# Kernel optimization log

Measured on AMD Instinct MI355X. Metric: run time of the kernel, lower is better.

The kernel has to match this reference:

```python
import jax, jax.numpy as jnp
import numpy as np

CLASSES = 10000
SMOOTHING = 0.1
COMPLEMENT = 1.0 - SMOOTHING
GAMMA = 3.0
IGNORE_INDEX = -1


def setup_inputs() -> dict:
    key = jax.random.key(0)
    k1, k2 = jax.random.split(key)
    B, S, C = 16, 512, CLASSES
    logits = jax.random.normal(k1, (B, S, C), dtype=jnp.float32)
    target = jax.random.randint(k2, (B, S), 0, C, dtype=jnp.int64)
    return {"logits": logits, "target": target}


def reference(logits, target):
    # logits: [B, S, C], target: [B, S]
    mask = (target != IGNORE_INDEX)
    safe_t = jnp.where(mask, target, 0)
    # label smoothing: one_hot * (1 - smoothing) + smoothing / C
    oh = jax.nn.one_hot(safe_t, CLASSES, dtype=logits.dtype)
    smooth = oh * COMPLEMENT + SMOOTHING / CLASSES
    logs = jax.nn.log_softmax(logits, axis=-1)          # [B, S, C]
    pt = jnp.exp(logs)
    # focal-weighted smoothed cross-entropy per token
    per_tok = -jnp.sum((1.0 - pt) ** GAMMA * logs * smooth, axis=-1)  # [B, S]
    # mean over non-ignored tokens (matches masked-select then .mean())
    maskf = mask.astype(per_tok.dtype)
    return jnp.sum(per_tok * maskf) / jnp.sum(maskf)
```

## Files before the change

### kernel.cpp

```cpp
#include <hip/hip_runtime.h>
#include <math.h>

#define NCLASSES   10000
#define NCLASSES4  2500
#define NT         512
#define PT         5
#define IGNORE_INDEX (-1)

#define SMOOTH_UNIF  1e-5f
#define SMOOTH_COMPL 0.9f

__device__ __forceinline__ float blk_max(float v, float* red) {
    #pragma unroll
    for (int off = 32; off > 0; off >>= 1)
        v = fmaxf(v, __shfl_down(v, off, 64));
    if ((threadIdx.x & 63) == 0) red[threadIdx.x >> 6] = v;
    __syncthreads();
    if (threadIdx.x == 0) {
        float r = red[0];
        #pragma unroll
        for (int j = 1; j < NT / 64; j++) r = fmaxf(r, red[j]);
        red[0] = r;
    }
    __syncthreads();
    return red[0];
}

__device__ __forceinline__ float blk_sum(float v, float* red) {
    #pragma unroll
    for (int off = 32; off > 0; off >>= 1)
        v += __shfl_down(v, off, 64);
    if ((threadIdx.x & 63) == 0) red[threadIdx.x >> 6] = v;
    __syncthreads();
    if (threadIdx.x == 0) {
        float r = red[0];
        #pragma unroll
        for (int j = 1; j < NT / 64; j++) r += red[j];
        red[0] = r;
    }
    __syncthreads();
    return red[0];
}

__global__ __launch_bounds__(NT)
void focal_ce_token_kernel(const float* __restrict__ logits,
                           const int* __restrict__ target,
                           float* __restrict__ tok_loss,
                           float* __restrict__ tok_mask) {
    const int row = blockIdx.x;
    const int t = threadIdx.x;
    const float4* __restrict__ xrow4 =
        reinterpret_cast<const float4*>(logits + (size_t)row * NCLASSES);
    const int tgt = target[row];

    __shared__ float redA[NT / 64], redB[NT / 64], redC[NT / 64];
    __shared__ float s_xt;
    if (t == 0) s_xt = 0.0f;

    float4 v[PT];
    float m = -INFINITY;
    #pragma unroll
    for (int i = 0; i < PT; i++) {
        int idx4 = t + i * NT;
        if (idx4 < NCLASSES4) {
            v[i] = xrow4[idx4];
            m = fmaxf(m, fmaxf(fmaxf(v[i].x, v[i].y), fmaxf(v[i].z, v[i].w)));
        }
    }

    if (tgt >= 0) {
        const int idx4_t = tgt >> 2;
        if (t == (idx4_t & (NT - 1))) {
            const int it = idx4_t >> 9;
            const int c = tgt & 3;
            float xt = 0.0f;
            #pragma unroll
            for (int i = 0; i < PT; i++)
                if (i == it)
                    xt = (c == 0) ? v[i].x : (c == 1) ? v[i].y
                       : (c == 2) ? v[i].z : v[i].w;
            s_xt = xt;
        }
    }

    const float M = blk_max(m, redA);

    float zs = 0.0f;
    #pragma unroll
    for (int i = 0; i < PT; i++) {
        int idx4 = t + i * NT;
        if (idx4 < NCLASSES4) {
            zs += __expf(v[i].x - M);
            zs += __expf(v[i].y - M);
            zs += __expf(v[i].z - M);
            zs += __expf(v[i].w - M);
        }
    }
    const float Z = blk_sum(zs, redB);
    const float lse = M + __logf(Z);

    float ws = 0.0f;
    #pragma unroll
    for (int i = 0; i < PT; i++) {
        int idx4 = t + i * NT;
        if (idx4 < NCLASSES4) {
            {
                float ls = v[i].x - lse; float pt = __expf(ls);
                float om = 1.0f - pt;    ws += om * om * om * ls;
            }
            {
                float ls = v[i].y - lse; float pt = __expf(ls);
                float om = 1.0f - pt;    ws += om * om * om * ls;
            }
            {
                float ls = v[i].z - lse; float pt = __expf(ls);
                float om = 1.0f - pt;    ws += om * om * om * ls;
            }
            {
                float ls = v[i].w - lse; float pt = __expf(ls);
                float om = 1.0f - pt;    ws += om * om * om * ls;
            }
        }
    }
    const float W = blk_sum(ws, redC);

    if (t == 0) {
        if (tgt == IGNORE_INDEX) {
            tok_loss[row] = 0.0f;
            tok_mask[row] = 0.0f;
        } else {
            float ls_t = s_xt - lse;
            float pt_t = __expf(ls_t);
            float om_t = 1.0f - pt_t;
            float w_t = om_t * om_t * om_t * ls_t;
            tok_loss[row] = -(SMOOTH_UNIF * W + SMOOTH_COMPL * w_t);
            tok_mask[row] = 1.0f;
        }
    }
}

__global__ __launch_bounds__(256)
void finalize_kernel(const float* __restrict__ tok_loss,
                     const float* __restrict__ tok_mask,
                     float* __restrict__ out, int n_tok) {
    __shared__ double tmp_s[4], tmp_c[4];
    double s = 0.0, c = 0.0;
    for (int i = threadIdx.x; i < n_tok; i += 256) {
        s += (double)tok_loss[i];
        c += (double)tok_mask[i];
    }
    #pragma unroll
    for (int off = 32; off > 0; off >>= 1) {
        s += __shfl_down(s, off, 64);
        c += __shfl_down(c, off, 64);
    }
    int lane = threadIdx.x & 63, w = threadIdx.x >> 6;
    if (lane == 0) { tmp_s[w] = s; tmp_c[w] = c; }
    __syncthreads();
    if (threadIdx.x == 0) {
        double S = tmp_s[0] + tmp_s[1] + tmp_s[2] + tmp_s[3];
        double C = tmp_c[0] + tmp_c[1] + tmp_c[2] + tmp_c[3];
        out[0] = (float)(S / C);
    }
}

extern "C" void kernel_launch(void* const* d_in, const int* in_sizes, int n_in,
                              void* d_out, int out_size, void* d_ws, size_t ws_size,
                              hipStream_t stream) {
    const float* logits = (const float*)d_in[0];
    const int* target = (const int*)d_in[1];
    const int n_tok = in_sizes[1];

    float* tok_loss = (float*)d_ws;
    float* tok_mask = tok_loss + n_tok;

    focal_ce_token_kernel<<<n_tok, NT, 0, stream>>>(logits, target, tok_loss, tok_mask);
    finalize_kernel<<<1, 256, 0, stream>>>(tok_loss, tok_mask, (float*)d_out, n_tok);
}
```

Measured before the change: 435.3 us.

## Compute focal loss in one pass via fixed-shift exponential moment sums

Replaces the max, sum-exp and focal-weight passes with a single pass that accumulates seven moments (sums of x, u, u^2, u^3 and their x-weighted versions, with u = exp(x - 16)), then reconstructs the focal-weighted sum algebraically in double precision. This removes two block-wide reductions and barriers and halves the exponentials per element. Block size also changes to 256 threads. The fixed shift instead of a row max risks float overflow or underflow for logits far from the expected range.

```diff
diff --git a/kernel.cpp b/kernel.cpp
--- a/kernel.cpp
+++ b/kernel.cpp
@@ -3,46 +3,16 @@
 
 #define NCLASSES   10000
 #define NCLASSES4  2500
-#define NT         512
-#define PT         5
+#define NT         256
+#define PT         10
+#define NWAVES     (NT / 64)
 #define IGNORE_INDEX (-1)
 
 #define SMOOTH_UNIF  1e-5f
 #define SMOOTH_COMPL 0.9f
+#define MSHIFT       16.0f
 
-__device__ __forceinline__ float blk_max(float v, float* red) {
-    #pragma unroll
-    for (int off = 32; off > 0; off >>= 1)
-        v = fmaxf(v, __shfl_down(v, off, 64));
-    if ((threadIdx.x & 63) == 0) red[threadIdx.x >> 6] = v;
-    __syncthreads();
-    if (threadIdx.x == 0) {
-        float r = red[0];
-        #pragma unroll
-        for (int j = 1; j < NT / 64; j++) r = fmaxf(r, red[j]);
-        red[0] = r;
-    }
-    __syncthreads();
-    return red[0];
-}
-
-__device__ __forceinline__ float blk_sum(float v, float* red) {
-    #pragma unroll
-    for (int off = 32; off > 0; off >>= 1)
-        v += __shfl_down(v, off, 64);
-    if ((threadIdx.x & 63) == 0) red[threadIdx.x >> 6] = v;
-    __syncthreads();
-    if (threadIdx.x == 0) {
-        float r = red[0];
-        #pragma unroll
-        for (int j = 1; j < NT / 64; j++) r += red[j];
-        red[0] = r;
-    }
-    __syncthreads();
-    return red[0];
-}
-
-__global__ __launch_bounds__(NT)
+__global__ __launch_bounds__(NT, 8)
 void focal_ce_token_kernel(const float* __restrict__ logits,
                            const int* __restrict__ target,
                            float* __restrict__ tok_loss,
@@ -52,88 +22,79 @@
     const float4* __restrict__ xrow4 =
         reinterpret_cast<const float4*>(logits + (size_t)row * NCLASSES);
     const int tgt = target[row];
+    const int idx4_t = (tgt >= 0) ? (tgt >> 2) : -1;
 
-    __shared__ float redA[NT / 64], redB[NT / 64], redC[NT / 64];
+    __shared__ float red[NWAVES][8];
     __shared__ float s_xt;
-    if (t == 0) s_xt = 0.0f;
 
-    float4 v[PT];
-    float m = -INFINITY;
+    float s0 = 0.f, s1 = 0.f, s1x = 0.f, s2 = 0.f, s2x = 0.f, s3 = 0.f, s3x = 0.f;
+
+#define ACC(xv) {                                   \
+        float x_ = (xv);                            \
+        float u_  = __expf(x_ - MSHIFT);            \
+        float u2_ = u_ * u_;                        \
+        float u3_ = u2_ * u_;                       \
+        s0 += x_;                                   \
+        s1 += u_;  s2 += u2_;  s3 += u3_;           \
+        s1x = fmaf(u_,  x_, s1x);                   \
+        s2x = fmaf(u2_, x_, s2x);                   \
+        s3x = fmaf(u3_, x_, s3x);                   \
+    }
+
     #pragma unroll
     for (int i = 0; i < PT; i++) {
-        int idx4 = t + i * NT;
+        const int idx4 = t + i * NT;
         if (idx4 < NCLASSES4) {
-            v[i] = xrow4[idx4];
-            m = fmaxf(m, fmaxf(fmaxf(v[i].x, v[i].y), fmaxf(v[i].z, v[i].w)));
+            const float4 v = xrow4[idx4];
+            if (idx4 == idx4_t) {
+                const int c = tgt & 3;
+                s_xt = (c == 0) ? v.x : (c == 1) ? v.y : (c == 2) ? v.z : v.w;
+            }
+            ACC(v.x); ACC(v.y); ACC(v.z); ACC(v.w);
         }
     }
+#undef ACC
 
-    if (tgt >= 0) {
-        const int idx4_t = tgt >> 2;
-        if (t == (idx4_t & (NT - 1))) {
-            const int it = idx4_t >> 9;
-            const int c = tgt & 3;
-            float xt = 0.0f;
-            #pragma unroll
-            for (int i = 0; i < PT; i++)
-                if (i == it)
-                    xt = (c == 0) ? v[i].x : (c == 1) ? v[i].y
-                       : (c == 2) ? v[i].z : v[i].w;
-            s_xt = xt;
-        }
+    #pragma unroll
+    for (int off = 32; off > 0; off >>= 1) {
+        s0  += __shfl_down(s0,  off, 64);
+        s1  += __shfl_down(s1,  off, 64);
+        s1x += __shfl_down(s1x, off, 64);
+        s2  += __shfl_down(s2,  off, 64);
+        s2x += __shfl_down(s2x, off, 64);
+        s3  += __shfl_down(s3,  off, 64);
+        s3x += __shfl_down(s3x, off, 64);
     }
-
-    const float M = blk_max(m, redA);
-
-    float zs = 0.0f;
-    #pragma unroll
-    for (int i = 0; i < PT; i++) {
-        int idx4 = t + i * NT;
-        if (idx4 < NCLASSES4) {
-            zs += __expf(v[i].x - M);
-            zs += __expf(v[i].y - M);
-            zs += __expf(v[i].z - M);
-            zs += __expf(v[i].w - M);
-        }
+    const int lane = t & 63, w = t >> 6;
+    if (lane == 0) {
+        red[w][0] = s0;  red[w][1] = s1;  red[w][2] = s1x;
+        red[w][3] = s2;  red[w][4] = s2x; red[w][5] = s3;  red[w][6] = s3x;
     }
-    const float Z = blk_sum(zs, redB);
-    const float lse = M + __logf(Z);
-
-    float ws = 0.0f;
-    #pragma unroll
-    for (int i = 0; i < PT; i++) {
-        int idx4 = t + i * NT;
-        if (idx4 < NCLASSES4) {
-            {
-                float ls = v[i].x - lse; float pt = __expf(ls);
-                float om = 1.0f - pt;    ws += om * om * om * ls;
-            }
-            {
-                float ls = v[i].y - lse; float pt = __expf(ls);
-                float om = 1.0f - pt;    ws += om * om * om * ls;
-            }
-            {
-                float ls = v[i].z - lse; float pt = __expf(ls);
-                float om = 1.0f - pt;    ws += om * om * om * ls;
-            }
-            {
-                float ls = v[i].w - lse; float pt = __expf(ls);
-                float om = 1.0f - pt;    ws += om * om * om * ls;
-            }
-        }
-    }
-    const float W = blk_sum(ws, redC);
+    __syncthreads();
 
     if (t == 0) {
+        double S0 = 0, S1 = 0, S1x = 0, S2 = 0, S2x = 0, S3 = 0, S3x = 0;
+        #pragma unroll
+        for (int j = 0; j < NWAVES; j++) {
+            S0  += red[j][0]; S1  += red[j][1]; S1x += red[j][2];
+            S2  += red[j][3]; S2x += red[j][4]; S3  += red[j][5]; S3x += red[j][6];
+        }
         if (tgt == IGNORE_INDEX) {
             tok_loss[row] = 0.0f;
             tok_mask[row] = 0.0f;
         } else {
-            float ls_t = s_xt - lse;
-            float pt_t = __expf(ls_t);
-            float om_t = 1.0f - pt_t;
-            float w_t = om_t * om_t * om_t * ls_t;
-            tok_loss[row] = -(SMOOTH_UNIF * W + SMOOTH_COMPL * w_t);
+            const double Z   = S1;
+            const double lse = (double)MSHIFT + log(Z);
+            const double t1  = S0 - (double)NCLASSES * lse;
+            const double t2  = S1x / Z - lse;
+            const double t3  = (S2x - lse * S2) / (Z * Z);
+            const double t4  = (S3x - lse * S3) / (Z * Z * Z);
+            const double W   = t1 - 3.0 * t2 + 3.0 * t3 - t4;
+            const double ls_t = (double)s_xt - lse;
+            const double pt_t = exp(ls_t);
+            const double om   = 1.0 - pt_t;
+            const double w_t  = om * om * om * ls_t;
+            tok_loss[row] = (float)(-(SMOOTH_UNIF * W + SMOOTH_COMPL * w_t));
             tok_mask[row] = 1.0f;
         }
     }
```

Measured after the change: 437.1 us. Within noise of the previous version (+0.4%).
